# Performance work log

Measured on AMD Instinct MI355X. Metric: run time of the kernel, lower is better.

The kernel has to match this reference:

```python
import math
import jax, jax.numpy as jnp
import numpy as np

B, L, D_IN, H, NLAYER, FUT, MDIM = 16, 128, 8, 128, 2, 12, 2

def setup_inputs() -> dict:
    key = jax.random.key(0)
    ks = jax.random.split(key, 16)
    def rn(k, shape, scale=0.05):
        return jax.random.normal(k, shape, jnp.float32) * scale
    return {
        'history': jax.random.normal(ks[0], (B, L, D_IN), jnp.float32),
        'history_mask': jnp.ones((B, L), jnp.float32),
        'Wp': rn(ks[1], (D_IN, H)), 'bp': jnp.zeros((H,), jnp.float32),
        'We1': rn(ks[2], (NLAYER, 4, H)), 'be1': jnp.zeros((NLAYER, H), jnp.float32),
        'We2': rn(ks[3], (NLAYER, H, H)), 'be2': jnp.zeros((NLAYER, H), jnp.float32),
        'Wa1': rn(ks[4], (NLAYER, 3 * H, H)), 'ba1': jnp.zeros((NLAYER, H), jnp.float32),
        'wa2': rn(ks[5], (NLAYER, H)), 'ba2': jnp.zeros((NLAYER,), jnp.float32),
        'Wm1': rn(ks[6], (NLAYER, 2 * H, H)), 'bm1': jnp.zeros((NLAYER, H), jnp.float32),
        'Wm2': rn(ks[7], (NLAYER, H, H)), 'bm2': jnp.zeros((NLAYER, H), jnp.float32),
        'Wo1': rn(ks[8], (NLAYER, 2 * H, H)), 'bo1': jnp.zeros((NLAYER, H), jnp.float32),
        'Wo2': rn(ks[9], (NLAYER, H, H)), 'bo2': jnp.zeros((NLAYER, H), jnp.float32),
        'ln_g': jnp.ones((NLAYER, H), jnp.float32), 'ln_b': jnp.zeros((NLAYER, H), jnp.float32),
        'hg': jnp.ones((D_IN + H,), jnp.float32), 'hb': jnp.zeros((D_IN + H,), jnp.float32),
        'Wh1': rn(ks[10], (D_IN + H, H)), 'bh1': jnp.zeros((H,), jnp.float32),
        'Wh2': rn(ks[11], (H, FUT * MDIM)), 'bh2': jnp.zeros((FUT * MDIM,), jnp.float32),
    }

def _layer_norm(x, g, b):
    mu = jnp.mean(x, -1, keepdims=True)
    var = jnp.mean((x - mu) ** 2, -1, keepdims=True)
    return (x - mu) * jax.lax.rsqrt(var + 1e-5) * g + b

def _forward(history, history_mask, Wp, bp, We1, be1, We2, be2, Wa1, ba1, wa2, ba2,
             Wm1, bm1, Wm2, bm2, Wo1, bo1, Wo2, bo2, ln_g, ln_b, hg, hb, Wh1, bh1, Wh2, bh2):
    valid = history_mask > 0
    vm = valid.astype(jnp.float32)[..., None]
    ts = jnp.cumsum(jnp.maximum(history[..., 5], 0.0), axis=1)
    # edge features [B,L,L,4]: dist, dt/300, same_src, same_step
    lat, lon, src_flag = history[..., 0], history[..., 1], history[..., 6]
    dlat = lat[:, :, None] - lat[:, None, :]
    dlon = lon[:, :, None] - lon[:, None, :]
    dist = jnp.sqrt(dlat * dlat + dlon * dlon + 1e-8)
    dt = jnp.abs(ts[:, :, None] - ts[:, None, :]) / 300.0
    same_src = (src_flag[:, :, None] == src_flag[:, None, :]).astype(jnp.float32)
    same_step = jnp.broadcast_to(jnp.eye(L, dtype=jnp.float32), (B, L, L))
    edge_feat = jnp.stack([dist, dt, same_src, same_step], axis=-1)
    h = (history @ Wp + bp) * vm
    inv = 1.0 / math.sqrt(H)
    for l in range(NLAYER):
        eh = jax.nn.relu(edge_feat @ We1[l] + be1[l]) @ We2[l] + be2[l]  # [B,L,L,H]
        # att MLP on concat([src,dst,edge]) -> split first weight into blocks
        sa = h @ Wa1[l, :H]       # src term, varies over i
        da = h @ Wa1[l, H:2 * H]  # dst term, varies over j
        att_hid = jnp.tanh(sa[:, :, None, :] + da[:, None, :, :] + eh @ Wa1[l, 2 * H:] + ba1[l])
        att = (att_hid @ wa2[l] + ba2[l]) * inv  # [B,L,L]
        att = jnp.where(valid[:, None, :], att, -1e9)  # key invalid
        att = jnp.where(valid[:, :, None], att, -1e9)  # query invalid
        w = jax.nn.softmax(att, axis=-1)
        # msg MLP on concat([src, edge])
        msg = jax.nn.relu((h @ Wm1[l, :H])[:, :, None, :] + eh @ Wm1[l, H:] + bm1[l]) @ Wm2[l] + bm2[l]
        agg = jnp.einsum('bij,bijk->bik', w, msg)
        out = jax.nn.relu(h @ Wo1[l, :H] + agg @ Wo1[l, H:] + bo1[l]) @ Wo2[l] + bo2[l]
        h = _layer_norm(h + out, ln_g[l], ln_b[l]) * vm
    # decoder state: last valid step
    vc = jnp.clip(jnp.sum(history_mask, axis=1).astype(jnp.int32), 1, L)
    last = vc - 1
    bidx = jnp.arange(B)
    ds = jnp.concatenate([history[bidx, last], h[bidx, last]], axis=-1)
    x = _layer_norm(ds, hg, hb)
    pred = (jax.nn.relu(x @ Wh1 + bh1) @ Wh2 + bh2).reshape(B, FUT, MDIM)
    pred = jnp.nan_to_num(pred, nan=0.0, posinf=1e4, neginf=-1e4)
    return pred, h

def reference(history, history_mask, Wp, bp, We1, be1, We2, be2, Wa1, ba1, wa2, ba2,
              Wm1, bm1, Wm2, bm2, Wo1, bo1, Wo2, bo2, ln_g, ln_b, hg, hb, Wh1, bh1, Wh2, bh2):
    return _forward(history, history_mask, Wp, bp, We1, be1, We2, be2, Wa1, ba1, wa2, ba2,
                    Wm1, bm1, Wm2, bm2, Wo1, bo1, Wo2, bo2, ln_g, ln_b, hg, hb, Wh1, bh1, Wh2, bh2)
```

## Files before the change

### kernel.cpp

```cpp
#include <hip/hip_runtime.h>
#include <math.h>

#define BB 16
#define LL 128
#define D_IN 8
#define HH 128
#define NLAYER 2
#define FUT 12
#define MDIM 2

typedef __attribute__((ext_vector_type(8))) __bf16 bf16x8;
typedef __attribute__((ext_vector_type(8))) short short8v;
typedef __attribute__((ext_vector_type(4))) float f32x4;

#define MFMA_B16(A, B, C) __builtin_amdgcn_mfma_f32_16x16x32_bf16(A, B, C, 0, 0, 0)

static __device__ __forceinline__ short f2bf(float f) {
    union { float f; unsigned u; } v; v.f = f;
    unsigned r = v.u + 0x7FFFu + ((v.u >> 16) & 1u);
    return (short)(r >> 16);
}

static __device__ __forceinline__ float tanh_fast(float x) {
    float e = __expf(2.f * x);
    return 1.f - 2.f / (e + 1.f);
}

__global__ __launch_bounds__(256) void k_prep(const float* __restrict__ hist, const float* __restrict__ mask,
                                              const float* __restrict__ Wp, const float* __restrict__ bp,
                                              const float* __restrict__ We2, const float* __restrict__ be2,
                                              const float* __restrict__ Wa1, const float* __restrict__ ba1,
                                              const float* __restrict__ Wm1, const float* __restrict__ bm1,
                                              const float* __restrict__ Wo1, const float* __restrict__ Wm2,
                                              const float* __restrict__ Wo2,
                                              float* __restrict__ ts, float* __restrict__ h,
                                              short* __restrict__ AmT, short* __restrict__ MmT,
                                              float* __restrict__ ca, float* __restrict__ cm,
                                              short* __restrict__ WT4, short* __restrict__ WT3) {
    __shared__ float row[HH];
    const int bid = blockIdx.x, tid = threadIdx.x;
    const int NC = NLAYER * (HH + 1);
    if (bid < BB) {
        int b = bid;
        if (tid < LL) row[tid] = fmaxf(hist[(b * LL + tid) * D_IN + 5], 0.f);
        __syncthreads();
        for (int d = 1; d < LL; d <<= 1) {
            float add = (tid < LL && tid >= d) ? row[tid - d] : 0.f;
            __syncthreads();
            if (tid < LL) row[tid] += add;
            __syncthreads();
        }
        if (tid < LL) ts[b * LL + tid] = row[tid];
        int k = tid & (HH - 1);
        float wp_r[D_IN];
#pragma unroll
        for (int f = 0; f < D_IN; f++) wp_r[f] = Wp[f * HH + k];
        float bpk = bp[k];
        int jbase = tid >> 7;
        for (int e = 0; e < 64; e++) {
            int j = e * 2 + jbase;
            int bj = b * LL + j;
            const float* hr = hist + (size_t)bj * D_IN;
            float acc = bpk;
#pragma unroll
            for (int f = 0; f < D_IN; f++) acc += hr[f] * wp_r[f];
            h[(size_t)bj * HH + k] = acc * (mask[bj] > 0.f ? 1.f : 0.f);
        }
    } else if (bid < BB + NC) {
        int cb = bid - BB;
        int l = cb / (HH + 1);
        int p = cb % (HH + 1);
        const float* WaE = Wa1 + (size_t)(l * 3 * HH + 2 * HH) * HH;
        const float* WmE = Wm1 + (size_t)(l * 2 * HH + HH) * HH;
        if (tid < HH) row[tid] = (p < HH) ? We2[(size_t)(l * HH + p) * HH + tid] : be2[l * HH + tid];
        __syncthreads();
        if (tid < HH) {
            float a = 0.f, m = 0.f;
            for (int k = 0; k < HH; k++) { float w = row[k]; a += w * WaE[k * HH + tid]; m += w * WmE[k * HH + tid]; }
            if (p < HH) {
                AmT[(size_t)l * HH * HH + tid * HH + p] = f2bf(a);
                MmT[(size_t)l * HH * HH + tid * HH + p] = f2bf(m);
            } else {
                ca[l * HH + tid] = a + ba1[l * HH + tid];
                cm[l * HH + tid] = m + bm1[l * HH + tid];
            }
        }
    } else {
        int m7 = bid - BB - NC;
        int l = m7 / 7, m = m7 % 7;
        const float* src;
        switch (m) {
            case 0: src = Wa1 + (size_t)(l * 3 * HH) * HH; break;
            case 1: src = Wa1 + (size_t)(l * 3 * HH + HH) * HH; break;
            case 2: src = Wm1 + (size_t)(l * 2 * HH) * HH; break;
            case 3: src = Wo1 + (size_t)(l * 2 * HH) * HH; break;
            case 4: src = Wm2 + (size_t)l * HH * HH; break;
            case 5: src = Wo1 + (size_t)(l * 2 * HH + HH) * HH; break;
            default: src = Wo2 + (size_t)l * HH * HH; break;
        }
        short* dst = (m < 4) ? (WT4 + (size_t)(l * 4 + m) * HH * HH)
                             : (WT3 + (size_t)(l * 3 + (m - 4)) * HH * HH);
#pragma unroll 4
        for (int e = 0; e < 64; e++) {
            int idx = e * 256 + tid;
            int c = idx >> 7, kk = idx & (HH - 1);
            dst[c * HH + kk] = f2bf(src[kk * HH + c]);
        }
    }
}

__global__ __launch_bounds__(256) void k_pre(const float* __restrict__ h, const short* __restrict__ WT4,
                                             const float* __restrict__ ca, const float* __restrict__ cm,
                                             float* __restrict__ base_a, float* __restrict__ da,
                                             float* __restrict__ base_m, float* __restrict__ oa, int l) {
    __shared__ __align__(16) short hA[16][136];
    const int tid = threadIdx.x, lane = tid & 63, wv = tid >> 6;
    const int lo = lane & 15, g4 = lane >> 4;
    const int r0 = blockIdx.x * 16;
    {
        int row = tid >> 4, cc = (tid & 15) * 8;
        const float* hr = h + (size_t)(r0 + row) * HH + cc;
        short8v pk;
#pragma unroll
        for (int e = 0; e < 8; e++) pk[e] = f2bf(hr[e]);
        *(short8v*)&hA[row][cc] = pk;
    }
    __syncthreads();
    bf16x8 af[4];
#pragma unroll
    for (int ks = 0; ks < 4; ks++)
        af[ks] = *(const bf16x8*)&hA[lo][ks * 32 + g4 * 8];
    const short* Wl = WT4 + (size_t)(l * 4 + wv) * HH * HH;
    float* dst;
    const float* bias = nullptr;
    if (wv == 0) { dst = base_a; bias = ca + l * HH; }
    else if (wv == 1) dst = da;
    else if (wv == 2) { dst = base_m; bias = cm + l * HH; }
    else dst = oa;
#pragma unroll
    for (int ct = 0; ct < 8; ct++) {
        int col = ct * 16 + lo;
        bf16x8 Bf[4];
#pragma unroll
        for (int ks = 0; ks < 4; ks++)
            Bf[ks] = *(const bf16x8*)(Wl + (size_t)col * HH + ks * 32 + g4 * 8);
        f32x4 acc = (f32x4){0.f, 0.f, 0.f, 0.f};
#pragma unroll
        for (int ks = 0; ks < 4; ks++) acc = MFMA_B16(af[ks], Bf[ks], acc);
        float bv = bias ? bias[col] : 0.f;
#pragma unroll
        for (int rg = 0; rg < 4; rg++)
            dst[(size_t)(r0 + g4 * 4 + rg) * HH + col] = acc[rg] + bv;
    }
}

__global__ __launch_bounds__(512) void k_attn(
    const float* __restrict__ hist, const float* __restrict__ mask, const float* __restrict__ ts,
    const float* __restrict__ base_a_g, const float* __restrict__ base_m_g, const float* __restrict__ da,
    const short* __restrict__ AmT, const short* __restrict__ MmT,
    const float* __restrict__ wa2, const float* __restrict__ ba2,
    const float* __restrict__ We1, const float* __restrict__ be1,
    float* __restrict__ v_out, int l) {
    __shared__ __align__(16) short t_lds[LL][136];
    __shared__ __align__(16) float bufA[1024];
    __shared__ float w_lds[128];
    __shared__ float val_s[128], base_a[128], base_m[128], wa2_s[128];

    const int tid = threadIdx.x;
    const int lane = tid & 63;
    const int wv = tid >> 6;
    const int lo = lane & 15, g4 = lane >> 4;
    const int k0 = wv * 16 + lo;
    const int bi = blockIdx.x, b = bi >> 7, i = bi & (LL - 1);

    bf16x8 Bf[4];
#pragma unroll
    for (int ks = 0; ks < 4; ks++)
        Bf[ks] = *(const bf16x8*)(AmT + (size_t)l * HH * HH + (size_t)k0 * HH + ks * 32 + g4 * 8);

    bufA[tid] = We1[l * 4 * HH + tid];
    if (tid < LL) {
        val_s[tid] = mask[b * LL + tid];
        wa2_s[tid] = wa2[l * HH + tid];
        bufA[512 + tid] = be1[l * HH + tid];
        base_a[tid] = base_a_g[(size_t)bi * HH + tid];
        base_m[tid] = base_m_g[(size_t)bi * HH + tid];
    }
    __syncthreads();

    {
        int jj = tid & (LL - 1);
        int q4 = tid >> 7;
        const float* hri = hist + (size_t)(b * LL + i) * D_IN;
        const float* hrj = hist + (size_t)(b * LL + jj) * D_IN;
        float dlat = hri[0] - hrj[0], dlon = hri[1] - hrj[1];
        float ea = sqrtf(dlat * dlat + dlon * dlon + 1e-8f);
        float eb = fabsf(ts[b * LL + i] - ts[b * LL + jj]) * (1.f / 300.f);
        float ec = (hri[6] == hrj[6]) ? 1.f : 0.f;
        float ed = (jj == i) ? 1.f : 0.f;
#pragma unroll
        for (int pass = 0; pass < 4; pass++) {
            int r0 = (q4 + pass * 4) * 8;
            short8v pk;
#pragma unroll
            for (int hv = 0; hv < 2; hv++) {
                f32x4 wa = *(const f32x4*)&bufA[r0 + hv * 4];
                f32x4 wb = *(const f32x4*)&bufA[128 + r0 + hv * 4];
                f32x4 wc = *(const f32x4*)&bufA[256 + r0 + hv * 4];
                f32x4 wd = *(const f32x4*)&bufA[384 + r0 + hv * 4];
                f32x4 wbe = *(const f32x4*)&bufA[512 + r0 + hv * 4];
#pragma unroll
                for (int e = 0; e < 4; e++) {
                    float v = ea * wa[e] + eb * wb[e] + ec * wc[e] + ed * wd[e] + wbe[e];
                    pk[hv * 4 + e] = f2bf(fmaxf(v, 0.f));
                }
            }
            *(short8v*)&t_lds[jj][r0] = pk;
        }
    }

    f32x4 acc[8];
    const float* da_b = da + (size_t)(b * LL) * HH;
#pragma unroll
    for (int jt = 0; jt < 8; jt++)
#pragma unroll
        for (int rg = 0; rg < 4; rg++)
            acc[jt][rg] = da_b[(size_t)(jt * 16 + g4 * 4 + rg) * HH + k0];
    __syncthreads();

#pragma unroll
    for (int ks = 0; ks < 4; ks++) {
#pragma unroll
        for (int jh = 0; jh < 2; jh++) {
            bf16x8 tf[4];
#pragma unroll
            for (int m = 0; m < 4; m++)
                tf[m] = *(const bf16x8*)&t_lds[(jh * 4 + m) * 16 + lo][ks * 32 + g4 * 8];
#pragma unroll
            for (int m = 0; m < 4; m++)
                acc[jh * 4 + m] = MFMA_B16(tf[m], Bf[ks], acc[jh * 4 + m]);
        }
    }

#pragma unroll
    for (int ks = 0; ks < 4; ks++)
        Bf[ks] = *(const bf16x8*)(MmT + (size_t)l * HH * HH + (size_t)k0 * HH + ks * 32 + g4 * 8);

    {
        float ba0 = base_a[k0];
        float w0a = wa2_s[k0];
#pragma unroll
        for (int jt = 0; jt < 8; jt++) {
#pragma unroll
            for (int rg = 0; rg < 4; rg++) {
                float p = tanh_fast(acc[jt][rg] + ba0) * w0a;
                p += __shfl_xor(p, 1);
                p += __shfl_xor(p, 2);
                p += __shfl_xor(p, 4);
                p += __shfl_xor(p, 8);
                if (lo == 0) bufA[wv * LL + jt * 16 + g4 * 4 + rg] = p;
            }
        }
    }
    __syncthreads();

    {
        const float inv = 0.08838834764831845f;
        float ba2l = ba2[l];
        float vi = val_s[i];
        float a0 = ba2l, a1 = ba2l;
#pragma unroll
        for (int w = 0; w < 8; w++) {
            a0 += bufA[w * LL + lane];
            a1 += bufA[w * LL + 64 + lane];
        }
        a0 *= inv; a1 *= inv;
        if (!(val_s[lane] > 0.f) || !(vi > 0.f)) a0 = -1e9f;
        if (!(val_s[64 + lane] > 0.f) || !(vi > 0.f)) a1 = -1e9f;
        float m = fmaxf(a0, a1);
#pragma unroll
        for (int d = 1; d < 64; d <<= 1) m = fmaxf(m, __shfl_xor(m, d));
        float e0 = __expf(a0 - m), e1 = __expf(a1 - m);
        float s = e0 + e1;
#pragma unroll
        for (int d = 1; d < 64; d <<= 1) s += __shfl_xor(s, d);
        float rs = 1.f / s;
        w_lds[lane] = e0 * rs;
        w_lds[64 + lane] = e1 * rs;
    }

#pragma unroll
    for (int jt = 0; jt < 8; jt++)
#pragma unroll
        for (int rg = 0; rg < 4; rg++) acc[jt][rg] = 0.f;
#pragma unroll
    for (int ks = 0; ks < 4; ks++) {
#pragma unroll
        for (int jh = 0; jh < 2; jh++) {
            bf16x8 tf[4];
#pragma unroll
            for (int m = 0; m < 4; m++)
                tf[m] = *(const bf16x8*)&t_lds[(jh * 4 + m) * 16 + lo][ks * 32 + g4 * 8];
#pragma unroll
            for (int m = 0; m < 4; m++)
                acc[jh * 4 + m] = MFMA_B16(tf[m], Bf[ks], acc[jh * 4 + m]);
        }
    }

    {
        float bm0 = base_m[k0];
        float mac = 0.f;
#pragma unroll
        for (int jt = 0; jt < 8; jt++) {
            f32x4 wj4 = *(const f32x4*)&w_lds[jt * 16 + g4 * 4];
#pragma unroll
            for (int rg = 0; rg < 4; rg++)
                mac += wj4[rg] * fmaxf(acc[jt][rg] + bm0, 0.f);
        }
        mac += __shfl_xor(mac, 16);
        mac += __shfl_xor(mac, 32);
        if (g4 == 0) v_out[(size_t)bi * HH + k0] = mac;
    }
}

__global__ __launch_bounds__(256) void k_post(
    const float* __restrict__ v, const float* __restrict__ oa_in, const float* __restrict__ h,
    const float* __restrict__ mask, const short* __restrict__ WT3,
    const float* __restrict__ bm2, const float* __restrict__ bo1, const float* __restrict__ bo2,
    const float* __restrict__ ln_g, const float* __restrict__ ln_b,
    float* __restrict__ hout, float* __restrict__ hcopy, int l,
    int do_pre, const short* __restrict__ WT4, const float* __restrict__ ca, const float* __restrict__ cm,
    float* __restrict__ base_a, float* __restrict__ da, float* __restrict__ base_m, float* __restrict__ oa_out) {
    __shared__ __align__(16) short xA[16][136];
    __shared__ __align__(16) short iA[16][136];
    __shared__ float red[2][4][16];
    const int tid = threadIdx.x, lane = tid & 63, wv = tid >> 6;
    const int lo = lane & 15, g4 = lane >> 4;
    const int r0 = blockIdx.x * 16;

    float oaR[2][4], hR[2][4], vmR[4];
    float bm2R[2], bo1R[2], bo2R[2], gR[2], bR[2];
#pragma unroll
    for (int ct = 0; ct < 2; ct++) {
        int c = wv * 32 + ct * 16 + lo;
        bm2R[ct] = bm2[l * HH + c];
        bo1R[ct] = bo1[l * HH + c];
        bo2R[ct] = bo2[l * HH + c];
        gR[ct] = ln_g[l * HH + c];
        bR[ct] = ln_b[l * HH + c];
    }
#pragma unroll
    for (int rg = 0; rg < 4; rg++) {
        int r = r0 + g4 * 4 + rg;
        vmR[rg] = mask[r];
#pragma unroll
        for (int ct = 0; ct < 2; ct++) {
            int c = wv * 32 + ct * 16 + lo;
            oaR[ct][rg] = oa_in[(size_t)r * HH + c];
            hR[ct][rg] = h[(size_t)r * HH + c];
        }
    }

    {
        int row = tid >> 4, cc = (tid & 15) * 8;
        const float* vr = v + (size_t)(r0 + row) * HH + cc;
        short8v pk;
#pragma unroll
        for (int e = 0; e < 8; e++) pk[e] = f2bf(vr[e]);
        *(short8v*)&xA[row][cc] = pk;
    }
    __syncthreads();

    bf16x8 af[4], Bf[2][4];
    f32x4 acc[2];

    {
        const short* W = WT3 + (size_t)(l * 3 + 0) * HH * HH;
#pragma unroll
        for (int ks = 0; ks < 4; ks++) af[ks] = *(const bf16x8*)&xA[lo][ks * 32 + g4 * 8];
#pragma unroll
        for (int ct = 0; ct < 2; ct++) {
            int col = wv * 32 + ct * 16 + lo;
#pragma unroll
            for (int ks = 0; ks < 4; ks++)
                Bf[ct][ks] = *(const bf16x8*)(W + (size_t)col * HH + ks * 32 + g4 * 8);
        }
        acc[0] = (f32x4){0.f, 0.f, 0.f, 0.f};
        acc[1] = (f32x4){0.f, 0.f, 0.f, 0.f};
#pragma unroll
        for (int ks = 0; ks < 4; ks++) {
            acc[0] = MFMA_B16(af[ks], Bf[0][ks], acc[0]);
            acc[1] = MFMA_B16(af[ks], Bf[1][ks], acc[1]);
        }
#pragma unroll
        for (int ct = 0; ct < 2; ct++)
#pragma unroll
            for (int rg = 0; rg < 4; rg++)
                iA[g4 * 4 + rg][wv * 32 + ct * 16 + lo] = f2bf(acc[ct][rg] + bm2R[ct]);
    }
    __syncthreads();

    {
        const short* W = WT3 + (size_t)(l * 3 + 1) * HH * HH;
#pragma unroll
        for (int ks = 0; ks < 4; ks++) af[ks] = *(const bf16x8*)&iA[lo][ks * 32 + g4 * 8];
#pragma unroll
        for (int ct = 0; ct < 2; ct++) {
            int col = wv * 32 + ct * 16 + lo;
#pragma unroll
            for (int ks = 0; ks < 4; ks++)
                Bf[ct][ks] = *(const bf16x8*)(W + (size_t)col * HH + ks * 32 + g4 * 8);
        }
        acc[0] = (f32x4){0.f, 0.f, 0.f, 0.f};
        acc[1] = (f32x4){0.f, 0.f, 0.f, 0.f};
#pragma unroll
        for (int ks = 0; ks < 4; ks++) {
            acc[0] = MFMA_B16(af[ks], Bf[0][ks], acc[0]);
            acc[1] = MFMA_B16(af[ks], Bf[1][ks], acc[1]);
        }
        __syncthreads();
#pragma unroll
        for (int ct = 0; ct < 2; ct++)
#pragma unroll
            for (int rg = 0; rg < 4; rg++)
                xA[g4 * 4 + rg][wv * 32 + ct * 16 + lo] =
                    f2bf(fmaxf(acc[ct][rg] + oaR[ct][rg] + bo1R[ct], 0.f));
    }
    __syncthreads();

    float y[2][4];
    {
        const short* W = WT3 + (size_t)(l * 3 + 2) * HH * HH;
#pragma unroll
        for (int ks = 0; ks < 4; ks++) af[ks] = *(const bf16x8*)&xA[lo][ks * 32 + g4 * 8];
#pragma unroll
        for (int ct = 0; ct < 2; ct++) {
            int col = wv * 32 + ct * 16 + lo;
#pragma unroll
            for (int ks = 0; ks < 4; ks++)
                Bf[ct][ks] = *(const bf16x8*)(W + (size_t)col * HH + ks * 32 + g4 * 8);
        }
        acc[0] = (f32x4){0.f, 0.f, 0.f, 0.f};
        acc[1] = (f32x4){0.f, 0.f, 0.f, 0.f};
#pragma unroll
        for (int ks = 0; ks < 4; ks++) {
            acc[0] = MFMA_B16(af[ks], Bf[0][ks], acc[0]);
            acc[1] = MFMA_B16(af[ks], Bf[1][ks], acc[1]);
        }
#pragma unroll
        for (int ct = 0; ct < 2; ct++)
#pragma unroll
            for (int rg = 0; rg < 4; rg++)
                y[ct][rg] = acc[ct][rg] + bo2R[ct] + hR[ct][rg];
    }
#pragma unroll
    for (int rg = 0; rg < 4; rg++) {
        float s = y[0][rg] + y[1][rg];
        float s2 = y[0][rg] * y[0][rg] + y[1][rg] * y[1][rg];
#pragma unroll
        for (int d = 1; d < 16; d <<= 1) { s += __shfl_xor(s, d); s2 += __shfl_xor(s2, d); }
        if (lo == 0) {
            red[0][wv][g4 * 4 + rg] = s;
            red[1][wv][g4 * 4 + rg] = s2;
        }
    }
    __syncthreads();
#pragma unroll
    for (int rg = 0; rg < 4; rg++) {
        int rl = g4 * 4 + rg;
        float mu = (red[0][0][rl] + red[0][1][rl] + red[0][2][rl] + red[0][3][rl]) * (1.f / HH);
        float ex2 = (red[1][0][rl] + red[1][1][rl] + red[1][2][rl] + red[1][3][rl]) * (1.f / HH);
        float var = ex2 - mu * mu;
        float rs = rsqrtf(var + 1e-5f);
        float vm = vmR[rg] > 0.f ? 1.f : 0.f;
        int r = r0 + rl;
#pragma unroll
        for (int ct = 0; ct < 2; ct++) {
            int c = wv * 32 + ct * 16 + lo;
            float hv = ((y[ct][rg] - mu) * rs * gR[ct] + bR[ct]) * vm;
            hout[(size_t)r * HH + c] = hv;
            if (hcopy) hcopy[(size_t)r * HH + c] = hv;
            if (do_pre) xA[rl][c] = f2bf(hv);
        }
    }

    if (do_pre) {
        __syncthreads();
        bf16x8 af2[4];
#pragma unroll
        for (int ks = 0; ks < 4; ks++) af2[ks] = *(const bf16x8*)&xA[lo][ks * 32 + g4 * 8];
        int ln = l + 1;
        const short* Wl = WT4 + (size_t)(ln * 4 + wv) * HH * HH;
        float* dst;
        const float* bias = nullptr;
        if (wv == 0) { dst = base_a; bias = ca + ln * HH; }
        else if (wv == 1) dst = da;
        else if (wv == 2) { dst = base_m; bias = cm + ln * HH; }
        else dst = oa_out;
#pragma unroll
        for (int ct = 0; ct < 8; ct++) {
            int col = ct * 16 + lo;
            bf16x8 Bf2[4];
#pragma unroll
            for (int ks = 0; ks < 4; ks++)
                Bf2[ks] = *(const bf16x8*)(Wl + (size_t)col * HH + ks * 32 + g4 * 8);
            f32x4 a2 = (f32x4){0.f, 0.f, 0.f, 0.f};
#pragma unroll
            for (int ks = 0; ks < 4; ks++) a2 = MFMA_B16(af2[ks], Bf2[ks], a2);
            float bv = bias ? bias[col] : 0.f;
#pragma unroll
            for (int rg = 0; rg < 4; rg++)
                dst[(size_t)(r0 + g4 * 4 + rg) * HH + col] = a2[rg] + bv;
        }
    }
}

__global__ __launch_bounds__(HH) void k_dec(const float* __restrict__ hist, const float* __restrict__ mask,
                                            const float* __restrict__ h, const float* __restrict__ hg,
                                            const float* __restrict__ hb, const float* __restrict__ Wh1,
                                            const float* __restrict__ bh1, const float* __restrict__ Wh2,
                                            const float* __restrict__ bh2, float* __restrict__ out) {
    int b = blockIdx.x, t = threadIdx.x;
    const int N = D_IN + HH;
    __shared__ float red[HH], x_s[D_IN + HH], u_s[HH];
    red[t] = mask[b * LL + t];
    __syncthreads();
    for (int s = 64; s > 0; s >>= 1) { if (t < s) red[t] += red[t + s]; __syncthreads(); }
    int vc = (int)red[0];
    vc = min(max(vc, 1), LL);
    int last = vc - 1;
    __syncthreads();
    if (t < D_IN) x_s[t] = hist[(size_t)(b * LL + last) * D_IN + t];
    x_s[D_IN + t] = h[(size_t)(b * LL + last) * HH + t];
    __syncthreads();
    float ps = 0.f;
    for (int f = t; f < N; f += HH) ps += x_s[f];
    red[t] = ps;
    __syncthreads();
    for (int s = 64; s > 0; s >>= 1) { if (t < s) red[t] += red[t + s]; __syncthreads(); }
    float mu = red[0] / N;
    __syncthreads();
    ps = 0.f;
    for (int f = t; f < N; f += HH) { float d = x_s[f] - mu; ps += d * d; }
    red[t] = ps;
    __syncthreads();
    for (int s = 64; s > 0; s >>= 1) { if (t < s) red[t] += red[t + s]; __syncthreads(); }
    float var = red[0] / N;
    float rs = rsqrtf(var + 1e-5f);
    __syncthreads();
    for (int f = t; f < N; f += HH) x_s[f] = (x_s[f] - mu) * rs * hg[f] + hb[f];
    __syncthreads();
    float acc = bh1[t];
    for (int f = 0; f < N; f++) acc += x_s[f] * Wh1[f * HH + t];
    u_s[t] = fmaxf(acc, 0.f);
    __syncthreads();
    if (t < FUT * MDIM) {
        float o = bh2[t];
        for (int k = 0; k < HH; k++) o += u_s[k] * Wh2[k * FUT * MDIM + t];
        if (isnan(o)) o = 0.f;
        else if (isinf(o)) o = (o > 0.f) ? 1e4f : -1e4f;
        out[b * FUT * MDIM + t] = o;
    }
}

extern "C" void kernel_launch(void* const* d_in, const int* in_sizes, int n_in,
                              void* d_out, int out_size, void* d_ws, size_t ws_size,
                              hipStream_t stream) {
    const float* hist = (const float*)d_in[0];
    const float* mask = (const float*)d_in[1];
    const float* Wp  = (const float*)d_in[2];
    const float* bp  = (const float*)d_in[3];
    const float* We1 = (const float*)d_in[4];
    const float* be1 = (const float*)d_in[5];
    const float* We2 = (const float*)d_in[6];
    const float* be2 = (const float*)d_in[7];
    const float* Wa1 = (const float*)d_in[8];
    const float* ba1 = (const float*)d_in[9];
    const float* wa2 = (const float*)d_in[10];
    const float* ba2 = (const float*)d_in[11];
    const float* Wm1 = (const float*)d_in[12];
    const float* bm1 = (const float*)d_in[13];
    const float* Wm2 = (const float*)d_in[14];
    const float* bm2 = (const float*)d_in[15];
    const float* Wo1 = (const float*)d_in[16];
    const float* bo1 = (const float*)d_in[17];
    const float* Wo2 = (const float*)d_in[18];
    const float* bo2 = (const float*)d_in[19];
    const float* ln_g = (const float*)d_in[20];
    const float* ln_b = (const float*)d_in[21];
    const float* hg  = (const float*)d_in[22];
    const float* hb  = (const float*)d_in[23];
    const float* Wh1 = (const float*)d_in[24];
    const float* bh1 = (const float*)d_in[25];
    const float* Wh2 = (const float*)d_in[26];
    const float* bh2 = (const float*)d_in[27];
    float* out = (float*)d_out;

    float* ws = (float*)d_ws;
    float* ts_w   = ws; ws += BB * LL;
    float* h_w    = ws; ws += BB * LL * HH;
    float* da_w   = ws; ws += BB * LL * HH;
    float* ba_w   = ws; ws += BB * LL * HH;
    float* bm_w   = ws; ws += BB * LL * HH;
    float* oa_w   = ws; ws += BB * LL * HH;
    float* v_w    = ws; ws += BB * LL * HH;
    float* ca_w   = ws; ws += NLAYER * HH;
    float* cm_w   = ws; ws += NLAYER * HH;
    short* AmT_w  = (short*)ws; ws += NLAYER * HH * HH / 2;
    short* MmT_w  = (short*)ws; ws += NLAYER * HH * HH / 2;
    short* WT4_w  = (short*)ws; ws += NLAYER * 4 * HH * HH / 2;
    short* WT3_w  = (short*)ws; ws += NLAYER * 3 * HH * HH / 2;

    const int NPREP = BB + NLAYER * (HH + 1) + NLAYER * 7;
    k_prep<<<NPREP, 256, 0, stream>>>(hist, mask, Wp, bp, We2, be2, Wa1, ba1, Wm1, bm1,
                                      Wo1, Wm2, Wo2, ts_w, h_w, AmT_w, MmT_w, ca_w, cm_w, WT4_w, WT3_w);
    k_pre<<<BB * LL / 16, 256, 0, stream>>>(h_w, WT4_w, ca_w, cm_w, ba_w, da_w, bm_w, oa_w, 0);
    for (int l = 0; l < NLAYER; l++) {
        k_attn<<<BB * LL, 512, 0, stream>>>(hist, mask, ts_w, ba_w, bm_w, da_w, AmT_w, MmT_w,
                                            wa2, ba2, We1, be1, v_w, l);
        int do_pre = (l < NLAYER - 1) ? 1 : 0;
        float* hcopy = (l == NLAYER - 1) ? (out + BB * FUT * MDIM) : nullptr;
        k_post<<<BB * LL / 16, 256, 0, stream>>>(v_w, oa_w, h_w, mask, WT3_w, bm2, bo1, bo2,
                                                 ln_g, ln_b, h_w, hcopy, l,
                                                 do_pre, WT4_w, ca_w, cm_w, ba_w, da_w, bm_w, oa_w);
    }
    k_dec<<<BB, HH, 0, stream>>>(hist, mask, h_w, hg, hb, Wh1, bh1, Wh2, bh2, out);
}
```

Measured before the change: 283.7 us.

## Fuse decoder into post kernel, swizzle attention LDS, split prep and pre work

Removes the separate decoder kernel by computing the last-valid-row LayerNorm and MLP head inside the final k_post block that owns that row. In k_attn, the padded t_lds tile becomes an XOR-swizzled unpadded layout, per-thread base/wa2 values move to registers, and the MFMA accumulation is restructured into two halves of four tiles to cut register pressure. k_pre now uses twice as many blocks, each computing half the columns, and k_prep splits its K loop across all 256 threads. The fused decoder switches to single-pass E[x^2]-mu^2 variance, which changes numerics slightly.

```diff
diff --git a/kernel.cpp b/kernel.cpp
--- a/kernel.cpp
+++ b/kernel.cpp
@@ -38,6 +38,7 @@
                                               float* __restrict__ ca, float* __restrict__ cm,
                                               short* __restrict__ WT4, short* __restrict__ WT3) {
     __shared__ float row[HH];
+    __shared__ float pa[256], pm[256];
     const int bid = blockIdx.x, tid = threadIdx.x;
     const int NC = NLAYER * (HH + 1);
     if (bid < BB) {
@@ -72,11 +73,22 @@
         int p = cb % (HH + 1);
         const float* WaE = Wa1 + (size_t)(l * 3 * HH + 2 * HH) * HH;
         const float* WmE = Wm1 + (size_t)(l * 2 * HH + HH) * HH;
+        int q = tid & 127, kh = tid >> 7;
         if (tid < HH) row[tid] = (p < HH) ? We2[(size_t)(l * HH + p) * HH + tid] : be2[l * HH + tid];
         __syncthreads();
+        float a = 0.f, m = 0.f;
+        int kbase = kh * 64;
+        for (int k = 0; k < 64; k++) {
+            float w = row[kbase + k];
+            a += w * WaE[(size_t)(kbase + k) * HH + q];
+            m += w * WmE[(size_t)(kbase + k) * HH + q];
+        }
+        pa[tid] = a;
+        pm[tid] = m;
+        __syncthreads();
         if (tid < HH) {
-            float a = 0.f, m = 0.f;
-            for (int k = 0; k < HH; k++) { float w = row[k]; a += w * WaE[k * HH + tid]; m += w * WmE[k * HH + tid]; }
+            a = pa[tid] + pa[128 + tid];
+            m = pm[tid] + pm[128 + tid];
             if (p < HH) {
                 AmT[(size_t)l * HH * HH + tid * HH + p] = f2bf(a);
                 MmT[(size_t)l * HH * HH + tid * HH + p] = f2bf(m);
@@ -116,7 +128,8 @@
     __shared__ __align__(16) short hA[16][136];
     const int tid = threadIdx.x, lane = tid & 63, wv = tid >> 6;
     const int lo = lane & 15, g4 = lane >> 4;
-    const int r0 = blockIdx.x * 16;
+    const int rt = blockIdx.x >> 1, half = blockIdx.x & 1;
+    const int r0 = rt * 16;
     {
         int row = tid >> 4, cc = (tid & 15) * 8;
         const float* hr = h + (size_t)(r0 + row) * HH + cc;
@@ -130,16 +143,18 @@
 #pragma unroll
     for (int ks = 0; ks < 4; ks++)
         af[ks] = *(const bf16x8*)&hA[lo][ks * 32 + g4 * 8];
-    const short* Wl = WT4 + (size_t)(l * 4 + wv) * HH * HH;
+    const int mat = half * 2 + (wv & 1);
+    const int ctbase = (wv >> 1) * 4;
+    const short* Wl = WT4 + (size_t)(l * 4 + mat) * HH * HH;
     float* dst;
     const float* bias = nullptr;
-    if (wv == 0) { dst = base_a; bias = ca + l * HH; }
-    else if (wv == 1) dst = da;
-    else if (wv == 2) { dst = base_m; bias = cm + l * HH; }
+    if (mat == 0) { dst = base_a; bias = ca + l * HH; }
+    else if (mat == 1) dst = da;
+    else if (mat == 2) { dst = base_m; bias = cm + l * HH; }
     else dst = oa;
 #pragma unroll
-    for (int ct = 0; ct < 8; ct++) {
-        int col = ct * 16 + lo;
+    for (int cc2 = 0; cc2 < 4; cc2++) {
+        int col = (ctbase + cc2) * 16 + lo;
         bf16x8 Bf[4];
 #pragma unroll
         for (int ks = 0; ks < 4; ks++)
@@ -161,10 +176,10 @@
     const float* __restrict__ wa2, const float* __restrict__ ba2,
     const float* __restrict__ We1, const float* __restrict__ be1,
     float* __restrict__ v_out, int l) {
-    __shared__ __align__(16) short t_lds[LL][136];
+    __shared__ __align__(16) short t_lds[LL][LL];
     __shared__ __align__(16) float bufA[1024];
-    __shared__ float w_lds[128];
-    __shared__ float val_s[128], base_a[128], base_m[128], wa2_s[128];
+    __shared__ float w_lds[LL];
+    __shared__ float val_s[LL];
 
     const int tid = threadIdx.x;
     const int lane = tid & 63;
@@ -173,6 +188,11 @@
     const int k0 = wv * 16 + lo;
     const int bi = blockIdx.x, b = bi >> 7, i = bi & (LL - 1);
 
+    const float base_a_r = base_a_g[(size_t)bi * HH + k0];
+    const float base_m_r = base_m_g[(size_t)bi * HH + k0];
+    const float wa2_r = wa2[l * HH + k0];
+    const float ba2l = ba2[l];
+
     bf16x8 Bf[4];
 #pragma unroll
     for (int ks = 0; ks < 4; ks++)
@@ -181,10 +201,7 @@
     bufA[tid] = We1[l * 4 * HH + tid];
     if (tid < LL) {
         val_s[tid] = mask[b * LL + tid];
-        wa2_s[tid] = wa2[l * HH + tid];
         bufA[512 + tid] = be1[l * HH + tid];
-        base_a[tid] = base_a_g[(size_t)bi * HH + tid];
-        base_m[tid] = base_m_g[(size_t)bi * HH + tid];
     }
     __syncthreads();
 
@@ -198,75 +215,72 @@
         float eb = fabsf(ts[b * LL + i] - ts[b * LL + jj]) * (1.f / 300.f);
         float ec = (hri[6] == hrj[6]) ? 1.f : 0.f;
         float ed = (jj == i) ? 1.f : 0.f;
+        char* trow = (char*)t_lds + jj * 256;
+        int swz = (jj & 7) << 4;
 #pragma unroll
         for (int pass = 0; pass < 4; pass++) {
-            int r0 = (q4 + pass * 4) * 8;
+            int r0c = (q4 + pass * 4) * 8;
             short8v pk;
 #pragma unroll
             for (int hv = 0; hv < 2; hv++) {
-                f32x4 wa = *(const f32x4*)&bufA[r0 + hv * 4];
-                f32x4 wb = *(const f32x4*)&bufA[128 + r0 + hv * 4];
-                f32x4 wc = *(const f32x4*)&bufA[256 + r0 + hv * 4];
-                f32x4 wd = *(const f32x4*)&bufA[384 + r0 + hv * 4];
-                f32x4 wbe = *(const f32x4*)&bufA[512 + r0 + hv * 4];
+                f32x4 wa = *(const f32x4*)&bufA[r0c + hv * 4];
+                f32x4 wb = *(const f32x4*)&bufA[128 + r0c + hv * 4];
+                f32x4 wc = *(const f32x4*)&bufA[256 + r0c + hv * 4];
+                f32x4 wd = *(const f32x4*)&bufA[384 + r0c + hv * 4];
+                f32x4 wbe = *(const f32x4*)&bufA[512 + r0c + hv * 4];
 #pragma unroll
                 for (int e = 0; e < 4; e++) {
                     float v = ea * wa[e] + eb * wb[e] + ec * wc[e] + ed * wd[e] + wbe[e];
                     pk[hv * 4 + e] = f2bf(fmaxf(v, 0.f));
                 }
             }
-            *(short8v*)&t_lds[jj][r0] = pk;
-        }
-    }
-
-    f32x4 acc[8];
+            *(short8v*)(trow + ((r0c * 2) ^ swz)) = pk;
+        }
+    }
+    __syncthreads();
+
     const float* da_b = da + (size_t)(b * LL) * HH;
-#pragma unroll
-    for (int jt = 0; jt < 8; jt++)
-#pragma unroll
-        for (int rg = 0; rg < 4; rg++)
-            acc[jt][rg] = da_b[(size_t)(jt * 16 + g4 * 4 + rg) * HH + k0];
-    __syncthreads();
-
-#pragma unroll
-    for (int ks = 0; ks < 4; ks++) {
-#pragma unroll
-        for (int jh = 0; jh < 2; jh++) {
+    const int rswz = (lo & 7) << 4;
+
+#pragma unroll
+    for (int jh = 0; jh < 2; jh++) {
+        f32x4 acc[4];
+#pragma unroll
+        for (int m = 0; m < 4; m++)
+#pragma unroll
+            for (int rg = 0; rg < 4; rg++)
+                acc[m][rg] = da_b[(size_t)((jh * 4 + m) * 16 + g4 * 4 + rg) * HH + k0];
+#pragma unroll
+        for (int ks = 0; ks < 4; ks++) {
             bf16x8 tf[4];
 #pragma unroll
-            for (int m = 0; m < 4; m++)
-                tf[m] = *(const bf16x8*)&t_lds[(jh * 4 + m) * 16 + lo][ks * 32 + g4 * 8];
-#pragma unroll
-            for (int m = 0; m < 4; m++)
-                acc[jh * 4 + m] = MFMA_B16(tf[m], Bf[ks], acc[jh * 4 + m]);
-        }
-    }
-
-#pragma unroll
-    for (int ks = 0; ks < 4; ks++)
-        Bf[ks] = *(const bf16x8*)(MmT + (size_t)l * HH * HH + (size_t)k0 * HH + ks * 32 + g4 * 8);
-
-    {
-        float ba0 = base_a[k0];
-        float w0a = wa2_s[k0];
-#pragma unroll
-        for (int jt = 0; jt < 8; jt++) {
+            for (int m = 0; m < 4; m++) {
+                int row = (jh * 4 + m) * 16 + lo;
+                tf[m] = *(const bf16x8*)((const char*)t_lds + row * 256 + ((ks * 64 + g4 * 16) ^ rswz));
+            }
+#pragma unroll
+            for (int m = 0; m < 4; m++) acc[m] = MFMA_B16(tf[m], Bf[ks], acc[m]);
+        }
+#pragma unroll
+        for (int m = 0; m < 4; m++)
 #pragma unroll
             for (int rg = 0; rg < 4; rg++) {
-                float p = tanh_fast(acc[jt][rg] + ba0) * w0a;
+                float p = tanh_fast(acc[m][rg] + base_a_r) * wa2_r;
                 p += __shfl_xor(p, 1);
                 p += __shfl_xor(p, 2);
                 p += __shfl_xor(p, 4);
                 p += __shfl_xor(p, 8);
-                if (lo == 0) bufA[wv * LL + jt * 16 + g4 * 4 + rg] = p;
+                if (lo == 0) bufA[wv * LL + (jh * 4 + m) * 16 + g4 * 4 + rg] = p;
             }
-        }
-    }
+    }
+
+#pragma unroll
+    for (int ks = 0; ks < 4; ks++)
+        Bf[ks] = *(const bf16x8*)(MmT + (size_t)l * HH * HH + (size_t)k0 * HH + ks * 32 + g4 * 8);
     __syncthreads();
 
     {
         const float inv = 0.08838834764831845f;
-        float ba2l = ba2[l];
         float vi = val_s[i];
         float a0 = ba2l, a1 = ba2l;
 #pragma unroll
@@ -289,38 +303,34 @@
         w_lds[64 + lane] = e1 * rs;
     }
 
-#pragma unroll
-    for (int jt = 0; jt < 8; jt++)
-#pragma unroll
-        for (int rg = 0; rg < 4; rg++) acc[jt][rg] = 0.f;
-#pragma unroll
-    for (int ks = 0; ks < 4; ks++) {
-#pragma unroll
-        for (int jh = 0; jh < 2; jh++) {
+    float mac = 0.f;
+#pragma unroll
+    for (int jh = 0; jh < 2; jh++) {
+        f32x4 acc[4];
+#pragma unroll
+        for (int m = 0; m < 4; m++) acc[m] = (f32x4){0.f, 0.f, 0.f, 0.f};
+#pragma unroll
+        for (int ks = 0; ks < 4; ks++) {
             bf16x8 tf[4];
 #pragma unroll
-            for (int m = 0; m < 4; m++)
-                tf[m] = *(const bf16x8*)&t_lds[(jh * 4 + m) * 16 + lo][ks * 32 + g4 * 8];
-#pragma unroll
-            for (int m = 0; m < 4; m++)
-                acc[jh * 4 + m] = MFMA_B16(tf[m], Bf[ks], acc[jh * 4 + m]);
-        }
-    }
-
-    {
-        float bm0 = base_m[k0];
-        float mac = 0.f;
-#pragma unroll
-        for (int jt = 0; jt < 8; jt++) {
-            f32x4 wj4 = *(const f32x4*)&w_lds[jt * 16 + g4 * 4];
+            for (int m = 0; m < 4; m++) {
+                int row = (jh * 4 + m) * 16 + lo;
+                tf[m] = *(const bf16x8*)((const char*)t_lds + row * 256 + ((ks * 64 + g4 * 16) ^ rswz));
+            }
+#pragma unroll
+            for (int m = 0; m < 4; m++) acc[m] = MFMA_B16(tf[m], Bf[ks], acc[m]);
+        }
+#pragma unroll
+        for (int m = 0; m < 4; m++) {
+            f32x4 wj4 = *(const f32x4*)&w_lds[(jh * 4 + m) * 16 + g4 * 4];
 #pragma unroll
             for (int rg = 0; rg < 4; rg++)
-                mac += wj4[rg] * fmaxf(acc[jt][rg] + bm0, 0.f);
-        }
-        mac += __shfl_xor(mac, 16);
-        mac += __shfl_xor(mac, 32);
-        if (g4 == 0) v_out[(size_t)bi * HH + k0] = mac;
-    }
+                mac += wj4[rg] * fmaxf(acc[m][rg] + base_m_r, 0.f);
+        }
+    }
+    mac += __shfl_xor(mac, 16);
+    mac += __shfl_xor(mac, 32);
+    if (g4 == 0) v_out[(size_t)bi * HH + k0] = mac;
 }
 
 __global__ __launch_bounds__(256) void k_post(
@@ -330,10 +340,15 @@
     const float* __restrict__ ln_g, const float* __restrict__ ln_b,
     float* __restrict__ hout, float* __restrict__ hcopy, int l,
     int do_pre, const short* __restrict__ WT4, const float* __restrict__ ca, const float* __restrict__ cm,
-    float* __restrict__ base_a, float* __restrict__ da, float* __restrict__ base_m, float* __restrict__ oa_out) {
+    float* __restrict__ base_a, float* __restrict__ da, float* __restrict__ base_m, float* __restrict__ oa_out,
+    const float* __restrict__ hist, const float* __restrict__ hg, const float* __restrict__ hb,
+    const float* __restrict__ Wh1, const float* __restrict__ bh1,
+    const float* __restrict__ Wh2, const float* __restrict__ bh2, float* __restrict__ dec_out) {
     __shared__ __align__(16) short xA[16][136];
     __shared__ __align__(16) short iA[16][136];
     __shared__ float red[2][4][16];
+    __shared__ float ln_row[HH];
+    __shared__ float dec_x[D_IN + HH];
     const int tid = threadIdx.x, lane = tid & 63, wv = tid >> 6;
     const int lo = lane & 15, g4 = lane >> 4;
     const int r0 = blockIdx.x * 16;
@@ -361,6 +376,14 @@
         }
     }
 
+    int lastRow = -1;
+    if (hcopy) {
+        float mv = (tid < LL) ? mask[(r0 >> 7) * LL + tid] : 0.f;
+#pragma unroll
+        for (int d = 1; d < 64; d <<= 1) mv += __shfl_xor(mv, d);
+        if (lane == 0) red[0][wv][0] = mv;
+    }
+
     {
         int row = tid >> 4, cc = (tid & 15) * 8;
         const float* vr = v + (size_t)(r0 + row) * HH + cc;
@@ -370,6 +393,12 @@
         *(short8v*)&xA[row][cc] = pk;
     }
     __syncthreads();
+
+    if (hcopy) {
+        int vc = (int)(red[0][0][0] + red[0][1][0] + red[0][2][0] + red[0][3][0]);
+        vc = min(max(vc, 1), LL);
+        lastRow = (r0 & ~(LL - 1)) + vc - 1;
+    }
 
     bf16x8 af[4], Bf[2][4];
     f32x4 acc[2];
@@ -481,6 +510,7 @@
             hout[(size_t)r * HH + c] = hv;
             if (hcopy) hcopy[(size_t)r * HH + c] = hv;
             if (do_pre) xA[rl][c] = f2bf(hv);
+            if (lastRow >= 0 && r == lastRow) ln_row[c] = hv;
         }
     }
 
@@ -513,53 +543,38 @@
                 dst[(size_t)(r0 + g4 * 4 + rg) * HH + col] = a2[rg] + bv;
         }
     }
-}
-
-__global__ __launch_bounds__(HH) void k_dec(const float* __restrict__ hist, const float* __restrict__ mask,
-                                            const float* __restrict__ h, const float* __restrict__ hg,
-                                            const float* __restrict__ hb, const float* __restrict__ Wh1,
-                                            const float* __restrict__ bh1, const float* __restrict__ Wh2,
-                                            const float* __restrict__ bh2, float* __restrict__ out) {
-    int b = blockIdx.x, t = threadIdx.x;
-    const int N = D_IN + HH;
-    __shared__ float red[HH], x_s[D_IN + HH], u_s[HH];
-    red[t] = mask[b * LL + t];
-    __syncthreads();
-    for (int s = 64; s > 0; s >>= 1) { if (t < s) red[t] += red[t + s]; __syncthreads(); }
-    int vc = (int)red[0];
-    vc = min(max(vc, 1), LL);
-    int last = vc - 1;
-    __syncthreads();
-    if (t < D_IN) x_s[t] = hist[(size_t)(b * LL + last) * D_IN + t];
-    x_s[D_IN + t] = h[(size_t)(b * LL + last) * HH + t];
-    __syncthreads();
-    float ps = 0.f;
-    for (int f = t; f < N; f += HH) ps += x_s[f];
-    red[t] = ps;
-    __syncthreads();
-    for (int s = 64; s > 0; s >>= 1) { if (t < s) red[t] += red[t + s]; __syncthreads(); }
-    float mu = red[0] / N;
-    __syncthreads();
-    ps = 0.f;
-    for (int f = t; f < N; f += HH) { float d = x_s[f] - mu; ps += d * d; }
-    red[t] = ps;
-    __syncthreads();
-    for (int s = 64; s > 0; s >>= 1) { if (t < s) red[t] += red[t + s]; __syncthreads(); }
-    float var = red[0] / N;
-    float rs = rsqrtf(var + 1e-5f);
-    __syncthreads();
-    for (int f = t; f < N; f += HH) x_s[f] = (x_s[f] - mu) * rs * hg[f] + hb[f];
-    __syncthreads();
-    float acc = bh1[t];
-    for (int f = 0; f < N; f++) acc += x_s[f] * Wh1[f * HH + t];
-    u_s[t] = fmaxf(acc, 0.f);
-    __syncthreads();
-    if (t < FUT * MDIM) {
-        float o = bh2[t];
-        for (int k = 0; k < HH; k++) o += u_s[k] * Wh2[k * FUT * MDIM + t];
-        if (isnan(o)) o = 0.f;
-        else if (isinf(o)) o = (o > 0.f) ? 1e4f : -1e4f;
-        out[b * FUT * MDIM + t] = o;
+
+    if (hcopy && lastRow >= r0 && lastRow < r0 + 16) {
+        const int N = D_IN + HH;
+        __syncthreads();
+        if (tid < D_IN) dec_x[tid] = hist[(size_t)lastRow * D_IN + tid];
+        if (tid < HH) dec_x[D_IN + tid] = ln_row[tid];
+        __syncthreads();
+        float px = (tid < N) ? dec_x[tid] : 0.f;
+        float px2 = px * px;
+#pragma unroll
+        for (int d = 1; d < 64; d <<= 1) { px += __shfl_xor(px, d); px2 += __shfl_xor(px2, d); }
+        if (lane == 0) { red[0][wv][0] = px; red[1][wv][0] = px2; }
+        __syncthreads();
+        float mu = (red[0][0][0] + red[0][1][0] + red[0][2][0] + red[0][3][0]) / (float)N;
+        float ex2 = (red[1][0][0] + red[1][1][0] + red[1][2][0] + red[1][3][0]) / (float)N;
+        float var = ex2 - mu * mu;
+        float rs = rsqrtf(var + 1e-5f);
+        if (tid < N) dec_x[tid] = (dec_x[tid] - mu) * rs * hg[tid] + hb[tid];
+        __syncthreads();
+        if (tid < HH) {
+            float a = bh1[tid];
+            for (int f = 0; f < N; f++) a += dec_x[f] * Wh1[(size_t)f * HH + tid];
+            ln_row[tid] = fmaxf(a, 0.f);
+        }
+        __syncthreads();
+        if (tid < FUT * MDIM) {
+            float o = bh2[tid];
+            for (int k = 0; k < HH; k++) o += ln_row[k] * Wh2[(size_t)k * FUT * MDIM + tid];
+            if (isnan(o)) o = 0.f;
+            else if (isinf(o)) o = (o > 0.f) ? 1e4f : -1e4f;
+            dec_out[(r0 >> 7) * FUT * MDIM + tid] = o;
+        }
     }
 }
 
@@ -614,7 +629,7 @@
     const int NPREP = BB + NLAYER * (HH + 1) + NLAYER * 7;
     k_prep<<<NPREP, 256, 0, stream>>>(hist, mask, Wp, bp, We2, be2, Wa1, ba1, Wm1, bm1,
                                       Wo1, Wm2, Wo2, ts_w, h_w, AmT_w, MmT_w, ca_w, cm_w, WT4_w, WT3_w);
-    k_pre<<<BB * LL / 16, 256, 0, stream>>>(h_w, WT4_w, ca_w, cm_w, ba_w, da_w, bm_w, oa_w, 0);
+    k_pre<<<BB * LL / 16 * 2, 256, 0, stream>>>(h_w, WT4_w, ca_w, cm_w, ba_w, da_w, bm_w, oa_w, 0);
     for (int l = 0; l < NLAYER; l++) {
         k_attn<<<BB * LL, 512, 0, stream>>>(hist, mask, ts_w, ba_w, bm_w, da_w, AmT_w, MmT_w,
                                             wa2, ba2, We1, be1, v_w, l);
@@ -622,7 +637,7 @@
         float* hcopy = (l == NLAYER - 1) ? (out + BB * FUT * MDIM) : nullptr;
         k_post<<<BB * LL / 16, 256, 0, stream>>>(v_w, oa_w, h_w, mask, WT3_w, bm2, bo1, bo2,
                                                  ln_g, ln_b, h_w, hcopy, l,
-                                                 do_pre, WT4_w, ca_w, cm_w, ba_w, da_w, bm_w, oa_w);
-    }
-    k_dec<<<BB, HH, 0, stream>>>(hist, mask, h_w, hg, hb, Wh1, bh1, Wh2, bh2, out);
+                                                 do_pre, WT4_w, ca_w, cm_w, ba_w, da_w, bm_w, oa_w,
+                                                 hist, hg, hb, Wh1, bh1, Wh2, bh2, out);
+    }
 }
```

Result: faster. 268.4 us (-5.4%).
